# Kernel optimization log

Measured on AMD Instinct MI355X. Metric: run time of the kernel, lower is better.

The kernel has to match this reference:

```python
import jax, jax.numpy as jnp
import numpy as np

C = 256          # conv_channels
C1 = C // 2      # 128
C2 = C // 4      # 64
G = 1            # relation_glimpse


def setup_inputs() -> dict:
    key = jax.random.key(0)
    ks = jax.random.split(key, 20)
    bs, Nr, in_dim, q_dim = 4, 256, 2052, 1024
    d_in = in_dim + 4  # pos (first 4 coords) re-appended
    s = 0.02
    inp = {
        "Q": jax.random.normal(ks[0], (bs, q_dim), jnp.float32),
        "X": jax.random.normal(ks[1], (bs, Nr, in_dim), jnp.float32),
        "Wv": jax.random.normal(ks[2], (d_in, C), jnp.float32) * s,
        "bv": jnp.zeros((C,), jnp.float32),
        "Wq": jax.random.normal(ks[3], (q_dim, C), jnp.float32) * s,
        "bq": jnp.zeros((C,), jnp.float32),
        # branch 0 (r_conv01/02/03): 1x1 convs == per-position dense
        "W01": jax.random.normal(ks[4], (C, C1), jnp.float32) * s,
        "b01": jnp.zeros((C1,), jnp.float32),
        "W02": jax.random.normal(ks[5], (C1, C2), jnp.float32) * s,
        "b02": jnp.zeros((C2,), jnp.float32),
        "W03": jax.random.normal(ks[6], (C2, G), jnp.float32) * s,
        "b03": jnp.zeros((G,), jnp.float32),
        # branch 1 (r_conv1/2/3): dilation on 1x1 kernels is a no-op
        "W1": jax.random.normal(ks[7], (C, C1), jnp.float32) * s,
        "b1": jnp.zeros((C1,), jnp.float32),
        "W2": jax.random.normal(ks[8], (C1, C2), jnp.float32) * s,
        "b2": jnp.zeros((C2,), jnp.float32),
        "W3": jax.random.normal(ks[9], (C2, G), jnp.float32) * s,
        "b3": jnp.zeros((G,), jnp.float32),
    }
    return inp


def _mlp3(P, Wa, ba, Wb, bb, Wc, bc):
    # P: [bs, Nr, Nr, C]; three 1x1-conv layers, ReLU after each (incl. last).
    h = jax.nn.relu(jnp.einsum("bijc,ck->bijk", P, Wa) + ba)
    h = jax.nn.relu(jnp.einsum("bijc,ck->bijk", h, Wb) + bb)
    h = jax.nn.relu(jnp.einsum("bijc,ck->bijk", h, Wc) + bc)
    return h[..., 0]  # [bs, Nr, Nr] (relation_glimpse == 1)


def _attn_map(h):
    # symmetrize, then softmax over all Nr*Nr positions
    s = h + jnp.swapaxes(h, 1, 2)
    bs, Nr, _ = s.shape
    return jax.nn.softmax(s.reshape(bs, Nr * Nr), axis=-1).reshape(bs, Nr, Nr)


def reference(Q, X, Wv, bv, Wq, bq, W01, b01, W02, b02, W03, b03,
              W1, b1, W2, b2, W3, b3):
    X_ = X
    # append pos (first 4 coords) -> [bs, Nr, in_dim+4]
    Xcat = jnp.concatenate([X, X[:, :, :4]], axis=2)
    Xp = jnp.einsum("bnd,dc->bnc", Xcat, Wv) + bv
    Qp = Q @ Wq + bq
    Xp = Xp + Qp[:, None, :]                       # [bs, Nr, C]
    P = Xp[:, None, :, :] * Xp[:, :, None, :]      # [bs, Nr, Nr, C] pairwise product
    m0 = _attn_map(_mlp3(P, W01, b01, W02, b02, W03, b03))
    m1 = _attn_map(_mlp3(P, W1, b1, W2, b2, W3, b3))
    # weighted aggregation with original features; /(2*glimpse), then sum over Nr
    rel = jnp.einsum("bij,bjd->bid", m0 + m1, X_) / (2.0 * G)
    return rel.sum(axis=1)  # [bs, in_dim]
```

## Files before the change

### kernel.cpp

```cpp
#include <hip/hip_runtime.h>
#include <hip/hip_bf16.h>

typedef __attribute__((ext_vector_type(8)))  short short8;
typedef __attribute__((ext_vector_type(4)))  float f32x4;
typedef __attribute__((ext_vector_type(16))) float f32x16;

#define NR 256
#define CC 256

__device__ __forceinline__ unsigned short f2bf(float x) {
    union { float f; unsigned int u; } v; v.f = x;
    unsigned int r = v.u + 0x7FFFu + ((v.u >> 16) & 1u);
    return (unsigned short)(r >> 16);
}

__device__ __forceinline__ unsigned int pk2bf(float a, float b) {
    __hip_bfloat162 h = __float22bfloat162_rn(make_float2(a, b));
    union { __hip_bfloat162 h; unsigned int u; } cv; cv.h = h;
    return cv.u;
}

__global__ __launch_bounds__(256) void setup_kernel(
    const float* __restrict__ Q, const float* __restrict__ Wq, float* __restrict__ Qpp,
    const float* __restrict__ Wv, unsigned short* __restrict__ wvp,
    const float* __restrict__ W01, const float* __restrict__ W1,
    const float* __restrict__ W02, const float* __restrict__ W2,
    unsigned short* __restrict__ wpa, unsigned short* __restrict__ wpb)
{
    __shared__ float tile[32][260];
    __shared__ float qs[256];
    const int bx = blockIdx.x;
    const int tid = threadIdx.x;

    if (bx < 16) {
        int ksl = bx & 3, b = bx >> 2;
        qs[tid] = Q[b * 1024 + ksl * 256 + tid];
        __syncthreads();
        float acc = 0.f;
        #pragma unroll 4
        for (int d = 0; d < 256; ++d) acc += qs[d] * Wq[(size_t)(ksl * 256 + d) * 256 + tid];
        Qpp[(ksl * 4 + b) * 256 + tid] = acc;
    } else if (bx < 81) {
        int ks = bx - 16;
        for (int idx = tid; idx < 32 * 256; idx += 256) {
            int cr = idx >> 8, n = idx & 255;
            int c = ks * 32 + cr;
            tile[cr][n] = (c < 2056) ? Wv[(size_t)c * 256 + n] : 0.f;
        }
        __syncthreads();
        #pragma unroll
        for (int q = 0; q < 4; ++q) {
            int t2 = tid * 4 + q;
            int nt = t2 >> 6, l = t2 & 63;
            int gg = l >> 4, jj = l & 15;
            short8 s;
            #pragma unroll
            for (int e = 0; e < 8; ++e)
                s[e] = (short)f2bf(tile[gg * 8 + e][nt * 16 + jj]);
            *(short8*)&wvp[((size_t)(ks * 16 + nt) * 64 + l) * 8] = s;
        }
    } else {
        int t = (bx - 81) * 256 + tid;
        if (t < 65536) {
            int e = t & 7, l = (t >> 3) & 63, ks = (t >> 9) & 15, nt = (t >> 13) & 3, br = (t >> 15) & 1;
            int cc = ks * 16 + (l >> 5) * 8 + e;
            int n = nt * 32 + (l & 31);
            const float* W = br ? W1 : W01;
            wpa[t] = f2bf(W[cc * 128 + n]);
        } else {
            int t2 = t - 65536;
            int e = t2 & 7, l = (t2 >> 3) & 63, ks = (t2 >> 9) & 7, nt = (t2 >> 12) & 1, br = (t2 >> 13) & 1;
            int cc = ks * 16 + (l >> 5) * 8 + e;
            int n = nt * 32 + (l & 31);
            const float* W = br ? W2 : W02;
            wpb[t2] = f2bf(W[cc * 64 + n]);
        }
    }
}

__global__ __launch_bounds__(512) void xp_kernel(
    const float* __restrict__ X, const unsigned short* __restrict__ wvp,
    const float* __restrict__ bv, const float* __restrict__ bq,
    const float* __restrict__ Qpp, float* __restrict__ Xp)
{
    __shared__ f32x4 red[8][2][65];
    const int tid = threadIdx.x;
    const int w = tid >> 6;
    const int lane = tid & 63;
    const int g = lane >> 4, j16 = lane & 15;
    const int mt = blockIdx.x;
    const int bn = blockIdx.y;
    const int b  = blockIdx.z;

    const int i0 = mt * 16;
    const int n0 = bn * 32;
    const float* xrow = X + ((size_t)(b * NR) + (i0 + j16)) * 2052;

    f32x4 acc[2] = {};

    for (int ks = w; ks < 64; ks += 8) {
        const int c0 = ks * 32 + g * 8;
        float4 xa = *(const float4*)(xrow + c0);
        float4 xb = *(const float4*)(xrow + c0 + 4);
        union { short8 s; unsigned int u[4]; } af;
        af.u[0] = pk2bf(xa.x, xa.y);
        af.u[1] = pk2bf(xa.z, xa.w);
        af.u[2] = pk2bf(xb.x, xb.y);
        af.u[3] = pk2bf(xb.z, xb.w);
        #pragma unroll
        for (int nt = 0; nt < 2; ++nt) {
            short8 bf = ((const short8*)wvp)[(size_t)(ks * 16 + bn * 2 + nt) * 64 + lane];
            acc[nt] = __builtin_amdgcn_mfma_f32_16x16x32_bf16(af.s, bf, acc[nt], 0, 0, 0);
        }
    }
    if (w == 0) {
        float xv[8];
        #pragma unroll
        for (int e = 0; e < 8; ++e) {
            int q = g * 8 + e;
            int csrc = (q < 4) ? (2048 + q) : (q - 4);
            xv[e] = xrow[csrc];
        }
        union { short8 s; unsigned int u[4]; } af;
        af.u[0] = pk2bf(xv[0], xv[1]);
        af.u[1] = pk2bf(xv[2], xv[3]);
        af.u[2] = pk2bf(xv[4], xv[5]);
        af.u[3] = pk2bf(xv[6], xv[7]);
        #pragma unroll
        for (int nt = 0; nt < 2; ++nt) {
            short8 bf = ((const short8*)wvp)[(size_t)(64 * 16 + bn * 2 + nt) * 64 + lane];
            acc[nt] = __builtin_amdgcn_mfma_f32_16x16x32_bf16(af.s, bf, acc[nt], 0, 0, 0);
        }
    }
    #pragma unroll
    for (int nt = 0; nt < 2; ++nt) red[w][nt][lane] = acc[nt];
    __syncthreads();

    {
        int nt  = tid >> 8;
        int rem = tid & 255;
        int l   = rem & 63;
        int reg = (rem >> 6) & 3;
        float r = 0.f;
        #pragma unroll
        for (int ww = 0; ww < 8; ++ww) r += red[ww][nt][l][reg];
        int gg = l >> 4, jj = l & 15;
        int n = n0 + nt * 16 + jj;
        float base = bv[n] + bq[n] + Qpp[b * 256 + n] + Qpp[(4 + b) * 256 + n]
                   + Qpp[(8 + b) * 256 + n] + Qpp[(12 + b) * 256 + n];
        int row = i0 + gg * 4 + reg;
        Xp[((b * NR) + row) * CC + n] = r + base;
    }
}

__global__ __launch_bounds__(512, 1) void pairs_kernel(
    const float* __restrict__ Xp,
    const unsigned short* __restrict__ wpa,
    const unsigned short* __restrict__ wpb,
    const float* __restrict__ b01, const float* __restrict__ b02,
    const float* __restrict__ b03,
    const float* __restrict__ b1,  const float* __restrict__ b2,
    const float* __restrict__ b3,
    const float* __restrict__ W03, const float* __restrict__ W3,
    float* __restrict__ colpart, float* __restrict__ rowpart)
{
    __shared__ __align__(16) unsigned short lds_wa[32768];
    __shared__ __align__(16) unsigned short lds_wb[8192];
    __shared__ __align__(16) float lds_si[2048];
    __shared__ __align__(16) float lds_bias1[128];
    __shared__ __align__(16) float lds_bias2[64];
    __shared__ __align__(16) float lds_w3[64];
    __shared__ float lds_c[8][33];

    const int tid = threadIdx.x;
    const int wave = tid >> 6;
    const int lane = tid & 63;
    const int hi = lane >> 5;
    const int j32 = lane & 31;

    int bx = blockIdx.x;
    int b = bx / 160;
    int r = bx - b * 160;
    int br = r / 80;
    int u = r - br * 80;
    int k = 0, off = 0;
    while (k < 7) {
        int cnt = 4 * ((9 - k) / 2);
        if (u < off + cnt) break;
        off += cnt; ++k;
    }
    int rel = u - off;
    int bpi = (9 - k) / 2;
    int it8 = 4 * k + rel / bpi;
    int jt_a = k + 2 * (rel % bpi);

    const int i = it8 * 8 + wave;
    const int blk = br * 4 + b;

    *(float4*)&lds_si[wave * 256 + lane * 4] =
        *(const float4*)&Xp[((b * NR) + i) * CC + lane * 4];

    {
        const uint4* g1 = (const uint4*)(wpa + (size_t)br * 32768);
        uint4* s1 = (uint4*)lds_wa;
        #pragma unroll
        for (int kk = 0; kk < 8; ++kk) s1[kk * 512 + tid] = g1[kk * 512 + tid];
        const uint4* g2 = (const uint4*)(wpb + (size_t)br * 8192);
        uint4* s2 = (uint4*)lds_wb;
        #pragma unroll
        for (int kk = 0; kk < 2; ++kk) s2[kk * 512 + tid] = g2[kk * 512 + tid];
        if (tid < 128) lds_bias1[tid] = br ? b1[tid] : b01[tid];
        else if (tid < 192) lds_bias2[tid - 128] = br ? b2[tid - 128] : b02[tid - 128];
        else if (tid < 256) lds_w3[tid - 192] = br ? W3[tid - 192] : W03[tid - 192];
    }
    __syncthreads();
    const float b3v = br ? b3[0] : b03[0];
    const float* si = lds_si + wave * 256;

    for (int pj = 0; pj < 2; ++pj) {
        const int jt = jt_a + pj;
        if (jt >= 8) break;
        const int j0 = jt * 32;
        const int j = j0 + j32;

        const float* xr = Xp + ((size_t)(b * NR) + j) * CC;
        short8 bfr[16];
        #pragma unroll
        for (int ks = 0; ks < 16; ++ks) {
            const int c0 = ks * 16 + hi * 8;
            float4 xa = *(const float4*)(xr + c0);
            float4 xb = *(const float4*)(xr + c0 + 4);
            float4 sa = *(const float4*)(si + c0);
            float4 sb = *(const float4*)(si + c0 + 4);
            union { short8 s; unsigned int uu[4]; } f;
            f.uu[0] = pk2bf(xa.x * sa.x, xa.y * sa.y);
            f.uu[1] = pk2bf(xa.z * sa.z, xa.w * sa.w);
            f.uu[2] = pk2bf(xb.x * sb.x, xb.y * sb.y);
            f.uu[3] = pk2bf(xb.z * sb.z, xb.w * sb.w);
            bfr[ks] = f.s;
        }

        f32x16 acc2[2];
        #pragma unroll
        for (int nt = 0; nt < 2; ++nt) {
            #pragma unroll
            for (int q = 0; q < 4; ++q) {
                const float* bb = &lds_bias2[nt * 32 + q * 8 + hi * 4];
                acc2[nt][q * 4 + 0] = bb[0];
                acc2[nt][q * 4 + 1] = bb[1];
                acc2[nt][q * 4 + 2] = bb[2];
                acc2[nt][q * 4 + 3] = bb[3];
            }
        }

        #pragma unroll
        for (int t = 0; t < 4; ++t) {
            f32x16 acc1;
            #pragma unroll
            for (int q = 0; q < 4; ++q) {
                const float* bb = &lds_bias1[t * 32 + q * 8 + hi * 4];
                acc1[q * 4 + 0] = bb[0];
                acc1[q * 4 + 1] = bb[1];
                acc1[q * 4 + 2] = bb[2];
                acc1[q * 4 + 3] = bb[3];
            }
            #pragma unroll
            for (int ks = 0; ks < 16; ++ks) {
                short8 wf = ((const short8*)lds_wa)[(t * 16 + ks) * 64 + lane];
                acc1 = __builtin_amdgcn_mfma_f32_32x32x16_bf16(wf, bfr[ks], acc1, 0, 0, 0);
            }
            #pragma unroll
            for (int s = 0; s < 2; ++s) {
                const int bse = s * 8;
                float rA0 = fmaxf(acc1[bse + 0], 0.f), rA1 = fmaxf(acc1[bse + 1], 0.f);
                float rA2 = fmaxf(acc1[bse + 2], 0.f), rA3 = fmaxf(acc1[bse + 3], 0.f);
                float rB0 = fmaxf(acc1[bse + 4], 0.f), rB1 = fmaxf(acc1[bse + 5], 0.f);
                float rB2 = fmaxf(acc1[bse + 6], 0.f), rB3 = fmaxf(acc1[bse + 7], 0.f);
                unsigned int uA0 = pk2bf(rA0, rA1), uA1 = pk2bf(rA2, rA3);
                unsigned int uB0 = pk2bf(rB0, rB1), uB1 = pk2bf(rB2, rB3);
                unsigned int pA0 = __shfl_xor(uA0, 32, 64), pA1 = __shfl_xor(uA1, 32, 64);
                unsigned int pB0 = __shfl_xor(uB0, 32, 64), pB1 = __shfl_xor(uB1, 32, 64);
                union { short8 s8; unsigned int uu[4]; } B2;
                B2.uu[0] = hi ? pB0 : uA0;
                B2.uu[1] = hi ? pB1 : uA1;
                B2.uu[2] = hi ? uB0 : pA0;
                B2.uu[3] = hi ? uB1 : pA1;
                const int ks2 = 2 * t + s;
                short8 w20 = ((const short8*)lds_wb)[ks2 * 64 + lane];
                short8 w21 = ((const short8*)lds_wb)[(8 + ks2) * 64 + lane];
                acc2[0] = __builtin_amdgcn_mfma_f32_32x32x16_bf16(w20, B2.s8, acc2[0], 0, 0, 0);
                acc2[1] = __builtin_amdgcn_mfma_f32_32x32x16_bf16(w21, B2.s8, acc2[1], 0, 0, 0);
            }
        }

        float part = 0.f;
        #pragma unroll
        for (int nt = 0; nt < 2; ++nt) {
            #pragma unroll
            for (int q = 0; q < 4; ++q) {
                const float* wv = &lds_w3[nt * 32 + q * 8 + hi * 4];
                part += fmaxf(acc2[nt][q * 4 + 0], 0.f) * wv[0];
                part += fmaxf(acc2[nt][q * 4 + 1], 0.f) * wv[1];
                part += fmaxf(acc2[nt][q * 4 + 2], 0.f) * wv[2];
                part += fmaxf(acc2[nt][q * 4 + 3], 0.f) * wv[3];
            }
        }
        part += __shfl_xor(part, 32, 64);
        const float h3 = fmaxf(part + b3v, 0.f);
        const float E = __expf(2.f * h3);
        const float Ec = (j >= i) ? E : 0.f;
        float Er = (j >  i) ? E : 0.f;

        Er += __shfl_xor(Er, 1, 64);
        Er += __shfl_xor(Er, 2, 64);
        Er += __shfl_xor(Er, 4, 64);
        Er += __shfl_xor(Er, 8, 64);
        Er += __shfl_xor(Er, 16, 64);
        Er += __shfl_xor(Er, 32, 64);
        if (lane == 0)
            rowpart[((size_t)blk * NR + i) * 8 + jt] = 0.5f * Er;

        if (!hi) lds_c[wave][j32] = Ec;
        __syncthreads();
        if (tid < 32) {
            float c = 0.f;
            #pragma unroll
            for (int w2 = 0; w2 < 8; ++w2) c += lds_c[w2][tid];
            colpart[(size_t)blk * 4608 + 64 * jt * (jt + 1) + tid * (4 * jt + 4) + it8] = c;
        }
        __syncthreads();
    }
}

__global__ __launch_bounds__(256) void colsoft_final_kernel(
    const float* __restrict__ colpart, const float* __restrict__ rowpart,
    float* __restrict__ wn)
{
    const int blk = blockIdx.x;
    const int j = threadIdx.x;
    const int jt = j >> 5, j32l = j & 31;
    const int cnt = 4 * jt + 4;
    float cs = 0.f;
    const float* cp = colpart + (size_t)blk * 4608 + 64 * jt * (jt + 1) + j32l * cnt;
    for (int it2 = 0; it2 < cnt; ++it2) cs += cp[it2];
    const float* rp = rowpart + ((size_t)blk * NR + j) * 8;
    for (int q = jt; q < 8; ++q) cs += rp[q];

    __shared__ float red[256];
    red[j] = cs; __syncthreads();
    for (int s = 128; s > 0; s >>= 1) {
        if (j < s) red[j] += red[j + s];
        __syncthreads();
    }
    wn[blk * 256 + j] = cs / red[0];
}

__global__ __launch_bounds__(256) void agg_part_kernel(
    const float* __restrict__ X, const float* __restrict__ wn,
    float* __restrict__ apart)
{
    const int dc = blockIdx.x, b = blockIdx.y, jc = blockIdx.z;
    const int d = dc * 256 + threadIdx.x;
    __shared__ float wc[32];
    if (threadIdx.x < 32) {
        int j = jc * 32 + threadIdx.x;
        wc[threadIdx.x] = 0.5f * (wn[b * 256 + j] + wn[(4 + b) * 256 + j]);
    }
    __syncthreads();
    if (d < 2052) {
        const float* xp = X + (size_t)b * NR * 2052 + (size_t)jc * 32 * 2052 + d;
        float a0 = 0.f, a1 = 0.f, a2 = 0.f, a3 = 0.f;
        for (int rr = 0; rr < 32; rr += 4) {
            a0 += wc[rr + 0] * xp[(size_t)(rr + 0) * 2052];
            a1 += wc[rr + 1] * xp[(size_t)(rr + 1) * 2052];
            a2 += wc[rr + 2] * xp[(size_t)(rr + 2) * 2052];
            a3 += wc[rr + 3] * xp[(size_t)(rr + 3) * 2052];
        }
        apart[(size_t)(jc * 4 + b) * 2304 + d] = (a0 + a1) + (a2 + a3);
    }
}

__global__ __launch_bounds__(256) void agg_final_kernel(
    const float* __restrict__ apart, float* __restrict__ out)
{
    const int dc = blockIdx.x, b = blockIdx.y;
    const int d = dc * 256 + threadIdx.x;
    if (d < 2052) {
        float s = 0.f;
        #pragma unroll
        for (int jc = 0; jc < 8; ++jc) s += apart[(size_t)(jc * 4 + b) * 2304 + d];
        out[b * 2052 + d] = s;
    }
}

extern "C" void kernel_launch(void* const* d_in, const int* in_sizes, int n_in,
                              void* d_out, int out_size, void* d_ws, size_t ws_size,
                              hipStream_t stream) {
    const float* Q   = (const float*)d_in[0];
    const float* X   = (const float*)d_in[1];
    const float* Wv  = (const float*)d_in[2];
    const float* bv  = (const float*)d_in[3];
    const float* Wq  = (const float*)d_in[4];
    const float* bq  = (const float*)d_in[5];
    const float* W01 = (const float*)d_in[6];
    const float* b01 = (const float*)d_in[7];
    const float* W02 = (const float*)d_in[8];
    const float* b02 = (const float*)d_in[9];
    const float* W03 = (const float*)d_in[10];
    const float* b03 = (const float*)d_in[11];
    const float* W1  = (const float*)d_in[12];
    const float* b1  = (const float*)d_in[13];
    const float* W2  = (const float*)d_in[14];
    const float* b2  = (const float*)d_in[15];
    const float* W3  = (const float*)d_in[16];
    const float* b3  = (const float*)d_in[17];

    char* ws = (char*)d_ws;
    float* Xp   = (float*)(ws + 0);
    float* Qpp  = (float*)(ws + 1048576);
    float* wn   = (float*)(ws + 1064960);
    unsigned short* wpa = (unsigned short*)(ws + 1073152);
    unsigned short* wpb = (unsigned short*)(ws + 1204224);
    float* colpart = (float*)(ws + 1236992);
    float* rowpart = (float*)(ws + 1384448);
    unsigned short* wvp = (unsigned short*)(ws + 1236992);
    float* apart = (float*)(ws + 0);
    float* out = (float*)d_out;

    setup_kernel<<<401, 256, 0, stream>>>(Q, Wq, Qpp, Wv, wvp,
                                          W01, W1, W02, W2, wpa, wpb);
    xp_kernel<<<dim3(16, 8, 4), 512, 0, stream>>>(X, wvp, bv, bq, Qpp, Xp);
    pairs_kernel<<<640, 512, 0, stream>>>(Xp, wpa, wpb, b01, b02, b03,
                                          b1, b2, b3, W03, W3, colpart, rowpart);
    colsoft_final_kernel<<<8, 256, 0, stream>>>(colpart, rowpart, wn);
    agg_part_kernel<<<dim3(9, 4, 8), 256, 0, stream>>>(X, wn, apart);
    agg_final_kernel<<<dim3(9, 4), 256, 0, stream>>>(apart, out);
}
```

Measured before the change: 112.1 us.

## Interleave both j-tiles per block to share weight fragments and overlap MFMA chains

The per-block loop over two j tiles is replaced by a single pass that builds both tiles' bf16 B fragments up front and interleaves their MFMA chains. Each LDS weight fragment load is shared by two MFMAs, and the two independent accumulator chains can hide MFMA dependency latency. It also removes the second pair of block barriers by reducing both column tiles in one step. The cost is roughly double the register footprint (two 16-entry fragment arrays and two accumulator sets), which risks spilling. Blocks whose second tile is out of range now do that tile's work anyway and throw it away.

```diff
diff --git a/kernel.cpp b/kernel.cpp
--- a/kernel.cpp
+++ b/kernel.cpp
@@ -170,7 +170,7 @@
     __shared__ __align__(16) float lds_bias1[128];
     __shared__ __align__(16) float lds_bias2[64];
     __shared__ __align__(16) float lds_w3[64];
-    __shared__ float lds_c[8][33];
+    __shared__ float lds_c[2][8][33];
 
     const int tid = threadIdx.x;
     const int wave = tid >> 6;
@@ -196,6 +196,9 @@
 
     const int i = it8 * 8 + wave;
     const int blk = br * 4 + b;
+    const int jtA = jt_a;
+    const bool validB = (jt_a + 1) < 8;
+    const int jtB = validB ? jt_a + 1 : jt_a;
 
     *(float4*)&lds_si[wave * 256 + lane * 4] =
         *(const float4*)&Xp[((b * NR) + i) * CC + lane * 4];
@@ -217,118 +220,161 @@
     const float b3v = br ? b3[0] : b03[0];
     const float* si = lds_si + wave * 256;
 
-    for (int pj = 0; pj < 2; ++pj) {
-        const int jt = jt_a + pj;
-        if (jt >= 8) break;
-        const int j0 = jt * 32;
-        const int j = j0 + j32;
-
-        const float* xr = Xp + ((size_t)(b * NR) + j) * CC;
-        short8 bfr[16];
-        #pragma unroll
-        for (int ks = 0; ks < 16; ++ks) {
-            const int c0 = ks * 16 + hi * 8;
-            float4 xa = *(const float4*)(xr + c0);
-            float4 xb = *(const float4*)(xr + c0 + 4);
-            float4 sa = *(const float4*)(si + c0);
-            float4 sb = *(const float4*)(si + c0 + 4);
+    const float* xrA = Xp + ((size_t)(b * NR) + (jtA * 32 + j32)) * CC;
+    const float* xrB = Xp + ((size_t)(b * NR) + (jtB * 32 + j32)) * CC;
+    short8 bfrA[16], bfrB[16];
+    #pragma unroll
+    for (int ks = 0; ks < 16; ++ks) {
+        const int c0 = ks * 16 + hi * 8;
+        float4 sa = *(const float4*)(si + c0);
+        float4 sb = *(const float4*)(si + c0 + 4);
+        {
+            float4 xa = *(const float4*)(xrA + c0);
+            float4 xb = *(const float4*)(xrA + c0 + 4);
             union { short8 s; unsigned int uu[4]; } f;
             f.uu[0] = pk2bf(xa.x * sa.x, xa.y * sa.y);
             f.uu[1] = pk2bf(xa.z * sa.z, xa.w * sa.w);
             f.uu[2] = pk2bf(xb.x * sb.x, xb.y * sb.y);
             f.uu[3] = pk2bf(xb.z * sb.z, xb.w * sb.w);
-            bfr[ks] = f.s;
-        }
-
-        f32x16 acc2[2];
-        #pragma unroll
-        for (int nt = 0; nt < 2; ++nt) {
-            #pragma unroll
-            for (int q = 0; q < 4; ++q) {
-                const float* bb = &lds_bias2[nt * 32 + q * 8 + hi * 4];
-                acc2[nt][q * 4 + 0] = bb[0];
-                acc2[nt][q * 4 + 1] = bb[1];
-                acc2[nt][q * 4 + 2] = bb[2];
-                acc2[nt][q * 4 + 3] = bb[3];
-            }
-        }
-
-        #pragma unroll
-        for (int t = 0; t < 4; ++t) {
-            f32x16 acc1;
-            #pragma unroll
-            for (int q = 0; q < 4; ++q) {
-                const float* bb = &lds_bias1[t * 32 + q * 8 + hi * 4];
-                acc1[q * 4 + 0] = bb[0];
-                acc1[q * 4 + 1] = bb[1];
-                acc1[q * 4 + 2] = bb[2];
-                acc1[q * 4 + 3] = bb[3];
-            }
-            #pragma unroll
-            for (int ks = 0; ks < 16; ++ks) {
-                short8 wf = ((const short8*)lds_wa)[(t * 16 + ks) * 64 + lane];
-                acc1 = __builtin_amdgcn_mfma_f32_32x32x16_bf16(wf, bfr[ks], acc1, 0, 0, 0);
-            }
-            #pragma unroll
-            for (int s = 0; s < 2; ++s) {
-                const int bse = s * 8;
-                float rA0 = fmaxf(acc1[bse + 0], 0.f), rA1 = fmaxf(acc1[bse + 1], 0.f);
-                float rA2 = fmaxf(acc1[bse + 2], 0.f), rA3 = fmaxf(acc1[bse + 3], 0.f);
-                float rB0 = fmaxf(acc1[bse + 4], 0.f), rB1 = fmaxf(acc1[bse + 5], 0.f);
-                float rB2 = fmaxf(acc1[bse + 6], 0.f), rB3 = fmaxf(acc1[bse + 7], 0.f);
+            bfrA[ks] = f.s;
+        }
+        {
+            float4 xa = *(const float4*)(xrB + c0);
+            float4 xb = *(const float4*)(xrB + c0 + 4);
+            union { short8 s; unsigned int uu[4]; } f;
+            f.uu[0] = pk2bf(xa.x * sa.x, xa.y * sa.y);
+            f.uu[1] = pk2bf(xa.z * sa.z, xa.w * sa.w);
+            f.uu[2] = pk2bf(xb.x * sb.x, xb.y * sb.y);
+            f.uu[3] = pk2bf(xb.z * sb.z, xb.w * sb.w);
+            bfrB[ks] = f.s;
+        }
+    }
+
+    f32x16 acc2A[2], acc2B[2];
+    #pragma unroll
+    for (int nt = 0; nt < 2; ++nt) {
+        #pragma unroll
+        for (int q = 0; q < 4; ++q) {
+            const float* bb = &lds_bias2[nt * 32 + q * 8 + hi * 4];
+            acc2A[nt][q * 4 + 0] = bb[0]; acc2B[nt][q * 4 + 0] = bb[0];
+            acc2A[nt][q * 4 + 1] = bb[1]; acc2B[nt][q * 4 + 1] = bb[1];
+            acc2A[nt][q * 4 + 2] = bb[2]; acc2B[nt][q * 4 + 2] = bb[2];
+            acc2A[nt][q * 4 + 3] = bb[3]; acc2B[nt][q * 4 + 3] = bb[3];
+        }
+    }
+
+    #pragma unroll 1
+    for (int t = 0; t < 4; ++t) {
+        f32x16 accA, accB;
+        #pragma unroll
+        for (int q = 0; q < 4; ++q) {
+            const float* bb = &lds_bias1[t * 32 + q * 8 + hi * 4];
+            accA[q * 4 + 0] = bb[0]; accB[q * 4 + 0] = bb[0];
+            accA[q * 4 + 1] = bb[1]; accB[q * 4 + 1] = bb[1];
+            accA[q * 4 + 2] = bb[2]; accB[q * 4 + 2] = bb[2];
+            accA[q * 4 + 3] = bb[3]; accB[q * 4 + 3] = bb[3];
+        }
+        #pragma unroll
+        for (int ks = 0; ks < 16; ++ks) {
+            short8 wf = ((const short8*)lds_wa)[(t * 16 + ks) * 64 + lane];
+            accA = __builtin_amdgcn_mfma_f32_32x32x16_bf16(wf, bfrA[ks], accA, 0, 0, 0);
+            accB = __builtin_amdgcn_mfma_f32_32x32x16_bf16(wf, bfrB[ks], accB, 0, 0, 0);
+        }
+        #pragma unroll
+        for (int s = 0; s < 2; ++s) {
+            const int bse = s * 8;
+            union { short8 s8; unsigned int uu[4]; } B2A, B2B;
+            {
+                float rA0 = fmaxf(accA[bse + 0], 0.f), rA1 = fmaxf(accA[bse + 1], 0.f);
+                float rA2 = fmaxf(accA[bse + 2], 0.f), rA3 = fmaxf(accA[bse + 3], 0.f);
+                float rB0 = fmaxf(accA[bse + 4], 0.f), rB1 = fmaxf(accA[bse + 5], 0.f);
+                float rB2 = fmaxf(accA[bse + 6], 0.f), rB3 = fmaxf(accA[bse + 7], 0.f);
                 unsigned int uA0 = pk2bf(rA0, rA1), uA1 = pk2bf(rA2, rA3);
                 unsigned int uB0 = pk2bf(rB0, rB1), uB1 = pk2bf(rB2, rB3);
                 unsigned int pA0 = __shfl_xor(uA0, 32, 64), pA1 = __shfl_xor(uA1, 32, 64);
                 unsigned int pB0 = __shfl_xor(uB0, 32, 64), pB1 = __shfl_xor(uB1, 32, 64);
-                union { short8 s8; unsigned int uu[4]; } B2;
-                B2.uu[0] = hi ? pB0 : uA0;
-                B2.uu[1] = hi ? pB1 : uA1;
-                B2.uu[2] = hi ? uB0 : pA0;
-                B2.uu[3] = hi ? uB1 : pA1;
-                const int ks2 = 2 * t + s;
-                short8 w20 = ((const short8*)lds_wb)[ks2 * 64 + lane];
-                short8 w21 = ((const short8*)lds_wb)[(8 + ks2) * 64 + lane];
-                acc2[0] = __builtin_amdgcn_mfma_f32_32x32x16_bf16(w20, B2.s8, acc2[0], 0, 0, 0);
-                acc2[1] = __builtin_amdgcn_mfma_f32_32x32x16_bf16(w21, B2.s8, acc2[1], 0, 0, 0);
+                B2A.uu[0] = hi ? pB0 : uA0;
+                B2A.uu[1] = hi ? pB1 : uA1;
+                B2A.uu[2] = hi ? uB0 : pA0;
+                B2A.uu[3] = hi ? uB1 : pA1;
             }
-        }
-
-        float part = 0.f;
-        #pragma unroll
-        for (int nt = 0; nt < 2; ++nt) {
-            #pragma unroll
-            for (int q = 0; q < 4; ++q) {
-                const float* wv = &lds_w3[nt * 32 + q * 8 + hi * 4];
-                part += fmaxf(acc2[nt][q * 4 + 0], 0.f) * wv[0];
-                part += fmaxf(acc2[nt][q * 4 + 1], 0.f) * wv[1];
-                part += fmaxf(acc2[nt][q * 4 + 2], 0.f) * wv[2];
-                part += fmaxf(acc2[nt][q * 4 + 3], 0.f) * wv[3];
+            {
+                float rA0 = fmaxf(accB[bse + 0], 0.f), rA1 = fmaxf(accB[bse + 1], 0.f);
+                float rA2 = fmaxf(accB[bse + 2], 0.f), rA3 = fmaxf(accB[bse + 3], 0.f);
+                float rB0 = fmaxf(accB[bse + 4], 0.f), rB1 = fmaxf(accB[bse + 5], 0.f);
+                float rB2 = fmaxf(accB[bse + 6], 0.f), rB3 = fmaxf(accB[bse + 7], 0.f);
+                unsigned int uA0 = pk2bf(rA0, rA1), uA1 = pk2bf(rA2, rA3);
+                unsigned int uB0 = pk2bf(rB0, rB1), uB1 = pk2bf(rB2, rB3);
+                unsigned int pA0 = __shfl_xor(uA0, 32, 64), pA1 = __shfl_xor(uA1, 32, 64);
+                unsigned int pB0 = __shfl_xor(uB0, 32, 64), pB1 = __shfl_xor(uB1, 32, 64);
+                B2B.uu[0] = hi ? pB0 : uA0;
+                B2B.uu[1] = hi ? pB1 : uA1;
+                B2B.uu[2] = hi ? uB0 : pA0;
+                B2B.uu[3] = hi ? uB1 : pA1;
             }
-        }
-        part += __shfl_xor(part, 32, 64);
-        const float h3 = fmaxf(part + b3v, 0.f);
-        const float E = __expf(2.f * h3);
-        const float Ec = (j >= i) ? E : 0.f;
-        float Er = (j >  i) ? E : 0.f;
-
-        Er += __shfl_xor(Er, 1, 64);
-        Er += __shfl_xor(Er, 2, 64);
-        Er += __shfl_xor(Er, 4, 64);
-        Er += __shfl_xor(Er, 8, 64);
-        Er += __shfl_xor(Er, 16, 64);
-        Er += __shfl_xor(Er, 32, 64);
-        if (lane == 0)
-            rowpart[((size_t)blk * NR + i) * 8 + jt] = 0.5f * Er;
-
-        if (!hi) lds_c[wave][j32] = Ec;
-        __syncthreads();
-        if (tid < 32) {
+            const int ks2 = 2 * t + s;
+            short8 w20 = ((const short8*)lds_wb)[ks2 * 64 + lane];
+            short8 w21 = ((const short8*)lds_wb)[(8 + ks2) * 64 + lane];
+            acc2A[0] = __builtin_amdgcn_mfma_f32_32x32x16_bf16(w20, B2A.s8, acc2A[0], 0, 0, 0);
+            acc2B[0] = __builtin_amdgcn_mfma_f32_32x32x16_bf16(w20, B2B.s8, acc2B[0], 0, 0, 0);
+            acc2A[1] = __builtin_amdgcn_mfma_f32_32x32x16_bf16(w21, B2A.s8, acc2A[1], 0, 0, 0);
+            acc2B[1] = __builtin_amdgcn_mfma_f32_32x32x16_bf16(w21, B2B.s8, acc2B[1], 0, 0, 0);
+        }
+    }
+
+    float partA = 0.f, partB = 0.f;
+    #pragma unroll
+    for (int nt = 0; nt < 2; ++nt) {
+        #pragma unroll
+        for (int q = 0; q < 4; ++q) {
+            const float* wv = &lds_w3[nt * 32 + q * 8 + hi * 4];
+            partA += fmaxf(acc2A[nt][q * 4 + 0], 0.f) * wv[0];
+            partA += fmaxf(acc2A[nt][q * 4 + 1], 0.f) * wv[1];
+            partA += fmaxf(acc2A[nt][q * 4 + 2], 0.f) * wv[2];
+            partA += fmaxf(acc2A[nt][q * 4 + 3], 0.f) * wv[3];
+            partB += fmaxf(acc2B[nt][q * 4 + 0], 0.f) * wv[0];
+            partB += fmaxf(acc2B[nt][q * 4 + 1], 0.f) * wv[1];
+            partB += fmaxf(acc2B[nt][q * 4 + 2], 0.f) * wv[2];
+            partB += fmaxf(acc2B[nt][q * 4 + 3], 0.f) * wv[3];
+        }
+    }
+    partA += __shfl_xor(partA, 32, 64);
+    partB += __shfl_xor(partB, 32, 64);
+    const float hA = fmaxf(partA + b3v, 0.f);
+    const float hB = fmaxf(partB + b3v, 0.f);
+    const float EA = __expf(2.f * hA);
+    const float EB = __expf(2.f * hB);
+    const int jA = jtA * 32 + j32;
+    const int jB = jtB * 32 + j32;
+    const float EcA = (jA >= i) ? EA : 0.f;
+    const float EcB = (validB && jB >= i) ? EB : 0.f;
+    float ErA = (jA > i) ? EA : 0.f;
+    float ErB = (validB && jB > i) ? EB : 0.f;
+
+    #pragma unroll
+    for (int sh = 1; sh <= 32; sh <<= 1) {
+        ErA += __shfl_xor(ErA, sh, 64);
+        ErB += __shfl_xor(ErB, sh, 64);
+    }
+    if (lane == 0) {
+        rowpart[((size_t)blk * NR + i) * 8 + jtA] = 0.5f * ErA;
+        if (validB) rowpart[((size_t)blk * NR + i) * 8 + jtB] = 0.5f * ErB;
+    }
+
+    if (!hi) {
+        lds_c[0][wave][j32] = EcA;
+        lds_c[1][wave][j32] = EcB;
+    }
+    __syncthreads();
+    if (tid < 64) {
+        int tile = tid >> 5, col = tid & 31;
+        if (tile == 0 || validB) {
             float c = 0.f;
             #pragma unroll
-            for (int w2 = 0; w2 < 8; ++w2) c += lds_c[w2][tid];
-            colpart[(size_t)blk * 4608 + 64 * jt * (jt + 1) + tid * (4 * jt + 4) + it8] = c;
-        }
-        __syncthreads();
+            for (int w2 = 0; w2 < 8; ++w2) c += lds_c[tile][w2][col];
+            int jt = tile ? jtB : jtA;
+            colpart[(size_t)blk * 4608 + 64 * jt * (jt + 1) + col * (4 * jt + 4) + it8] = c;
+        }
     }
 }
 
```

After: 113.6 us. About the same (+1.3%).
